# Performance work log

Measured on AMD Instinct MI355X. Metric: run time of the kernel, lower is better.

Reference implementation:

```python
import jax, jax.numpy as jnp
import numpy as np

HIDDEN = 2048
HEADS = 16
HEAD_DIM = HIDDEN // HEADS
BATCH = 2
SEQ = 2048
ROPE_BASE = 10000.0


def _rope_cos_sin(seq_len, head_dim, dtype):
    inv_freq = 1.0 / (ROPE_BASE ** (jnp.arange(0, head_dim, 2, dtype=jnp.float32) / head_dim))
    t = jnp.arange(seq_len, dtype=jnp.float32)
    freqs = jnp.outer(t, inv_freq)                 # [S, D/2]
    emb = jnp.concatenate([freqs, freqs], axis=-1)  # [S, D]
    return jnp.cos(emb).astype(dtype), jnp.sin(emb).astype(dtype)


def _rotate_half(x):
    x1, x2 = jnp.split(x, 2, axis=-1)
    return jnp.concatenate([-x2, x1], axis=-1)


def setup_inputs() -> dict:
    key = jax.random.key(0)
    ks = jax.random.split(key, 5)
    scale = 1.0 / np.sqrt(HIDDEN)
    return {
        "x": jax.random.normal(ks[0], (BATCH, SEQ, HIDDEN), dtype=jnp.float32),
        "Wq": jax.random.normal(ks[1], (HIDDEN, HIDDEN), dtype=jnp.float32) * scale,
        "Wk": jax.random.normal(ks[2], (HIDDEN, HIDDEN), dtype=jnp.float32) * scale,
        "Wv": jax.random.normal(ks[3], (HIDDEN, HIDDEN), dtype=jnp.float32) * scale,
        "Wo": jax.random.normal(ks[4], (HIDDEN, HIDDEN), dtype=jnp.float32) * scale,
    }


def reference(x, Wq, Wk, Wv, Wo):
    B, S, H = x.shape
    # projections (torch Linear: y = x @ W.T)
    q = jnp.einsum('bsh,oh->bso', x, Wq).reshape(B, S, HEADS, HEAD_DIM).transpose(0, 2, 1, 3)
    k = jnp.einsum('bsh,oh->bso', x, Wk).reshape(B, S, HEADS, HEAD_DIM).transpose(0, 2, 1, 3)
    v = jnp.einsum('bsh,oh->bso', x, Wv).reshape(B, S, HEADS, HEAD_DIM).transpose(0, 2, 1, 3)
    # RoPE
    cos, sin = _rope_cos_sin(S, HEAD_DIM, x.dtype)  # [S, D]
    cos = cos[None, None]  # [1,1,S,D]
    sin = sin[None, None]
    q = q * cos + _rotate_half(q) * sin
    k = k * cos + _rotate_half(k) * sin
    # attention scores [B, H, S, S]
    scale = HEAD_DIM ** -0.5
    scores = jnp.einsum('bhqd,bhkd->bhqk', q, k) * scale
    causal = jnp.triu(jnp.ones((S, S), dtype=bool), k=1)  # kv_len==seq -> diagonal=1
    scores = jnp.where(causal[None, None], -jnp.inf, scores)
    attn = jax.nn.softmax(scores.astype(jnp.float32), axis=-1).astype(q.dtype)
    # dropout is identity in eval mode
    out = jnp.einsum('bhqk,bhkd->bhqd', attn, v)  # [B,H,S,D]
    out = out.transpose(0, 2, 1, 3).reshape(B, S, H)
    return jnp.einsum('bsh,oh->bso', out, Wo)
```

## Files before the change

kernel.cpp:

```cpp
#include <hip/hip_runtime.h>
#include <hip/hip_bf16.h>
#include <cstdint>
#include <cstddef>

constexpr int HIDDEN = 2048;
constexpr int HEADS  = 16;
constexpr int HD     = 128;
constexpr int BATCH  = 2;
constexpr int SEQ    = 2048;
constexpr int MROWS  = BATCH * SEQ;

typedef __attribute__((ext_vector_type(8))) short bf16x8;
typedef __attribute__((ext_vector_type(4))) float f32x4;
typedef __attribute__((ext_vector_type(4))) unsigned u32x4;

constexpr float QSCALE = 0.08838834764831845f * 1.4426950408889634f;

__device__ __forceinline__ unsigned short f2bf(float f) {
  union { float f; unsigned int u; } c; c.f = f;
  unsigned int r = c.u + 0x7FFFu + ((c.u >> 16) & 1u);
  return (unsigned short)(r >> 16);
}
__device__ __forceinline__ float bf2f(unsigned short u) {
  union { unsigned int u; float f; } c; c.u = ((unsigned int)u) << 16;
  return c.f;
}

__device__ __forceinline__ void gload_lds16(const void* g, void* l) {
  __builtin_amdgcn_global_load_lds(
      (const __attribute__((address_space(1))) void*)g,
      (__attribute__((address_space(3))) void*)l, 16, 0, 0);
}

__global__ void k_cvt_all(const float* __restrict__ x,
                          const float* __restrict__ w0, const float* __restrict__ w1,
                          const float* __restrict__ w2, const float* __restrict__ w3,
                          unsigned short* __restrict__ out) {
  constexpr int N4X = MROWS * HIDDEN / 4;
  constexpr int N4W = HIDDEN * HIDDEN / 4;
  int idx = blockIdx.x * 256 + threadIdx.x;
  const float* src;
  int off;
  if (idx < N4X) { src = x; off = idx; }
  else {
    int j = idx - N4X;
    int seg = j >> 20;
    off = j & (N4W - 1);
    src = (seg == 0) ? w0 : (seg == 1) ? w1 : (seg == 2) ? w2 : w3;
  }
  float4 v = reinterpret_cast<const float4*>(src)[off];
  ushort4 o;
  o.x = f2bf(v.x); o.y = f2bf(v.y); o.z = f2bf(v.z); o.w = f2bf(v.w);
  reinterpret_cast<ushort4*>(out)[idx] = o;
}

constexpr int GK  = 2048;
constexpr int GNT = GK / 64;

template<int MODE, int BM, int BN>
__global__ __launch_bounds__(512)
__attribute__((amdgpu_waves_per_eu(2)))
void k_gemm256(const unsigned short* __restrict__ A,
               const unsigned short* __restrict__ Bm,
               void* __restrict__ Cout) {
  constexpr int ABYTES = BM * 64 * 2;
  constexpr int BBYTES = BN * 64 * 2;
  constexpr int AG = BM / 64;
  constexpr int BG = BN / 64;
  constexpr int G  = AG + BG;
  constexpr int MI = BM / 32;
  constexpr int NI = BN / 64;

  __shared__ char lds[2 * (ABYTES + BBYTES)];
  char* ldsA = lds;
  char* ldsB = lds + 2 * ABYTES;

  const int t    = threadIdx.x;
  const int lane = t & 63;
  const int w    = t >> 6;
  const int wr   = w >> 2;
  const int wc   = w & 3;
  const int l15  = lane & 15, lg = lane >> 4;

  const int orig = blockIdx.x;
  const int wg   = (orig & 7) * 32 + (orig >> 3);
  const int m0   = (wg >> 4) * BM;
  const int n0   = (wg & 15) * BN;

  const int rowA = t >> 3;
  const int xsel = ((t & 7) ^ (rowA & 7)) * 8;
  const unsigned short* aS = A  + (size_t)(m0 + rowA) * GK + xsel;
  const unsigned short* bS = Bm + (size_t)(n0 + rowA) * GK + xsel;
  char* aD = ldsA + t * 16;
  char* bD = ldsB + t * 16;

#define STAGEG(buf, kt) do {                                       \
    const unsigned short* ap = aS + (kt) * 64;                     \
    const unsigned short* bp = bS + (kt) * 64;                     \
    char* ad = aD + (buf) * ABYTES;                                \
    char* bd = bD + (buf) * BBYTES;                                \
    _Pragma("unroll")                                              \
    for (int g = 0; g < AG; ++g)                                   \
      gload_lds16(ap + (size_t)g * 64 * GK, ad + g * 8192);        \
    _Pragma("unroll")                                              \
    for (int g = 0; g < BG; ++g)                                   \
      gload_lds16(bp + (size_t)g * 64 * GK, bd + g * 8192);        \
  } while (0)

  const int xr  = (l15 & 7) << 4;
  const int vo0 = (lg * 16) ^ xr;
  const int vo1 = (64 + lg * 16) ^ xr;
  const char* aR = ldsA + wr * (BM / 2) * 128 + l15 * 128;
  const char* bR = ldsB + wc * (BN / 4) * 128 + l15 * 128;

  f32x4 acc[MI][NI];
#pragma unroll
  for (int mi = 0; mi < MI; ++mi)
#pragma unroll
    for (int ni = 0; ni < NI; ++ni)
#pragma unroll
      for (int r = 0; r < 4; ++r) acc[mi][ni][r] = 0.f;

  STAGEG(0, 0);
  STAGEG(1, 1);
  asm volatile("s_waitcnt vmcnt(%0)" :: "i"(G) : "memory");
  __builtin_amdgcn_s_barrier();
  asm volatile("" ::: "memory");

#pragma unroll 1
  for (int kt = 0; kt < GNT; ++kt) {
    const int buf = kt & 1;
    const char* a = aR + buf * ABYTES;
    const char* b = bR + buf * BBYTES;

    bf16x8 af0[MI], bf0[NI];
#pragma unroll
    for (int mi = 0; mi < MI; ++mi)
      af0[mi] = *reinterpret_cast<const bf16x8*>(a + mi * 2048 + vo0);
#pragma unroll
    for (int ni = 0; ni < NI; ++ni)
      bf0[ni] = *reinterpret_cast<const bf16x8*>(b + ni * 2048 + vo0);
    __builtin_amdgcn_s_setprio(1);
#pragma unroll
    for (int mi = 0; mi < MI; ++mi)
#pragma unroll
      for (int ni = 0; ni < NI; ++ni)
        acc[mi][ni] = __builtin_amdgcn_mfma_f32_16x16x32_bf16(af0[mi], bf0[ni], acc[mi][ni], 0, 0, 0);
    __builtin_amdgcn_s_setprio(0);

    bf16x8 af1[MI], bf1[NI];
#pragma unroll
    for (int mi = 0; mi < MI; ++mi)
      af1[mi] = *reinterpret_cast<const bf16x8*>(a + mi * 2048 + vo1);
#pragma unroll
    for (int ni = 0; ni < NI; ++ni)
      bf1[ni] = *reinterpret_cast<const bf16x8*>(b + ni * 2048 + vo1);

    asm volatile("s_waitcnt lgkmcnt(0)" ::: "memory");
    __builtin_amdgcn_s_barrier();
    asm volatile("" ::: "memory");

    if (kt < GNT - 2) STAGEG(buf, kt + 2);

    __builtin_amdgcn_s_setprio(1);
#pragma unroll
    for (int mi = 0; mi < MI; ++mi)
#pragma unroll
      for (int ni = 0; ni < NI; ++ni)
        acc[mi][ni] = __builtin_amdgcn_mfma_f32_16x16x32_bf16(af1[mi], bf1[ni], acc[mi][ni], 0, 0, 0);
    __builtin_amdgcn_s_setprio(0);

    if (kt < GNT - 2) asm volatile("s_waitcnt vmcnt(%0)" :: "i"(G) : "memory");
    else              asm volatile("s_waitcnt vmcnt(0)" ::: "memory");
    __builtin_amdgcn_s_barrier();
    asm volatile("" ::: "memory");
  }
#undef STAGEG

  if (MODE == 0) {
    float* xch = reinterpret_cast<float*>(lds);
    const int lid = w * 64 + lane;
    const int pid = (w ^ 1) * 64 + lane;
#pragma unroll
    for (int half = 0; half < 2; ++half) {
      __syncthreads();
#pragma unroll
      for (int mi4 = 0; mi4 < 4; ++mi4)
#pragma unroll
        for (int ni = 0; ni < NI; ++ni)
#pragma unroll
          for (int r = 0; r < 4; ++r)
            xch[(mi4 * 16 + ni * 4 + r) * 512 + lid] = acc[half * 4 + mi4][ni][r];
      __syncthreads();
#pragma unroll
      for (int mi4 = 0; mi4 < 4; ++mi4) {
#pragma unroll
        for (int ni = 0; ni < NI; ++ni) {
          const int col  = n0 + wc * 64 + ni * 16 + l15;
          const float invf = exp2f((float)(col & 63) * -0.20762050593046868f);
#pragma unroll
          for (int r = 0; r < 4; ++r) {
            int row = m0 + wr * 128 + (half * 4 + mi4) * 16 + lg * 4 + r;
            int s = row & (SEQ - 1);
            float own = acc[half * 4 + mi4][ni][r];
            float oth = xch[(mi4 * 16 + ni * 4 + r) * 512 + pid];
            float sn, cs;
            __sincosf((float)s * invf, &sn, &cs);
            float outv = (wc & 1) ? (own * cs + oth * sn) : (own * cs - oth * sn);
            int bb = row >> 11;
            int which = col >> 11;
            int hc = col & 2047;
            int h = hc >> 7, d = hc & (HD - 1);
            if (which == 0) outv *= QSCALE;
            size_t addr = (size_t)which * ((size_t)MROWS * HIDDEN)
                        + ((size_t)(bb * HEADS + h) * SEQ + s) * HD + d;
            reinterpret_cast<unsigned short*>(Cout)[addr] = f2bf(outv);
          }
        }
      }
    }
  } else {
#pragma unroll
    for (int mi = 0; mi < MI; ++mi) {
#pragma unroll
      for (int ni = 0; ni < NI; ++ni) {
#pragma unroll
        for (int r = 0; r < 4; ++r) {
          int row = m0 + wr * (BM / 2) + mi * 16 + lg * 4 + r;
          int col = n0 + wc * (BN / 4) + ni * 16 + l15;
          float v = acc[mi][ni][r];
          if (MODE == 2) {
            reinterpret_cast<float*>(Cout)[(size_t)row * 2048 + col] = v;
          } else {
            int h = row >> 7, d = row & (HD - 1);
            int bb = col >> 11, s = col & (SEQ - 1);
            size_t addr = ((size_t)(bb * HEADS + h) * HD + d) * SEQ + s;
            reinterpret_cast<unsigned short*>(Cout)[addr] = f2bf(v);
          }
        }
      }
    }
  }
}

constexpr int QB  = 128;
constexpr int KVB = 64;
constexpr int NQT = SEQ / QB;

__global__ __launch_bounds__(512)
__attribute__((amdgpu_waves_per_eu(4, 4)))
void k_attn(const unsigned short* __restrict__ Q,
            const unsigned short* __restrict__ Kk,
            const unsigned short* __restrict__ Vt,
            unsigned short* __restrict__ O) {
  __shared__ char lds[2 * 16384 + 2 * 16384];
  char* Ks = lds;
  char* Vs = lds + 2 * 16384;

  const int t    = threadIdx.x;
  const int lane = t & 63;
  const int w    = t >> 6;
  const int l15  = lane & 15, lg = lane >> 4;

  const int lin     = blockIdx.x + 16 * blockIdx.y;
  const int pos     = lin >> 3;
  const int logical = (lin & 7) * 64 + pos;
  const int bh      = logical >> 4;
  const int qt0     = logical & 15;
  const int qt      = (pos < 32) ? qt0 : (15 - qt0);
  const int b  = bh >> 4, h = bh & 15;
  const int q0b  = qt * QB;
  const int q0w  = q0b + w * 16;
  const int qw_hi = q0w + 15;

  const unsigned short* Qb = Q  + (size_t)bh * SEQ * HD;
  const unsigned short* Kb = Kk + (size_t)bh * SEQ * HD;
  const unsigned short* Vb = Vt + (size_t)bh * HD * SEQ;

  bf16x8 qf[4];
#pragma unroll
  for (int c = 0; c < 4; ++c)
    qf[c] = *reinterpret_cast<const bf16x8*>(Qb + (size_t)(q0w + l15) * HD + c * 32 + lg * 8);

  float m = -1e30f, lpart = 0.f;
  f32x4 oacc[8];
#pragma unroll
  for (int dt = 0; dt < 8; ++dt)
#pragma unroll
    for (int r = 0; r < 4; ++r) oacc[dt][r] = 0.f;

  const int sp     = t * 16;
  const int srow   = sp >> 8;
  const int scolb  = (sp & 255) ^ ((srow & 7) << 4);
  const unsigned short* ksrc2 = Kb + (size_t)srow * HD + (scolb >> 1);
  char* kdst2 = Ks + sp;

  const int vrow  = t >> 3;
  const int vcolb = ((t & 7) << 4) ^ ((vrow & 7) << 4);
  const unsigned short* vsrc = Vb + (size_t)vrow * SEQ + (vcolb >> 1);
  char* vdst = Vs + t * 16;

  const int nb = q0b / KVB + 2;

  gload_lds16(ksrc2, kdst2);
  gload_lds16(ksrc2 + (size_t)32 * HD, kdst2 + 8192);
  gload_lds16(vsrc, vdst);
  gload_lds16(vsrc + (size_t)64 * SEQ, vdst + 8192);

  int cur = 0;
  for (int kb = 0; kb < nb; ++kb) {
    const int kv0 = kb * KVB;
    if (kb + 1 < nb) {
      const int nxt = kv0 + KVB;
      char* nk = kdst2 + (cur ^ 1) * 16384;
      char* nv = vdst  + (cur ^ 1) * 16384;
      gload_lds16(ksrc2 + (size_t)nxt * HD, nk);
      gload_lds16(ksrc2 + (size_t)(nxt + 32) * HD, nk + 8192);
      gload_lds16(vsrc + nxt, nv);
      gload_lds16(vsrc + (size_t)64 * SEQ + nxt, nv + 8192);
      asm volatile("s_waitcnt vmcnt(4)" ::: "memory");
    } else {
      asm volatile("s_waitcnt vmcnt(0)" ::: "memory");
    }
    __builtin_amdgcn_s_barrier();
    asm volatile("" ::: "memory");

    if (kv0 <= qw_hi) {
      const char* Kc = Ks + cur * 16384;
      const char* Vc = Vs + cur * 16384;
      f32x4 sc[4];
#pragma unroll
      for (int tt = 0; tt < 4; ++tt)
#pragma unroll
        for (int r = 0; r < 4; ++r) sc[tt][r] = 0.f;
      __builtin_amdgcn_s_setprio(1);
#pragma unroll
      for (int tt = 0; tt < 4; ++tt) {
        const int kr = tt * 16 + l15;
        const int xr = (kr & 7) << 4;
#pragma unroll
        for (int c = 0; c < 4; ++c) {
          bf16x8 kf = *reinterpret_cast<const bf16x8*>(
              Kc + kr * 256 + ((c * 64 + lg * 16) ^ xr));
          sc[tt] = __builtin_amdgcn_mfma_f32_16x16x32_bf16(kf, qf[c], sc[tt], 0, 0, 0);
        }
      }
      __builtin_amdgcn_s_setprio(0);

      const bool full = (kv0 + KVB - 1 <= q0w);
      const int qg = q0w + l15;
      if (!full) {
        const int kvb = kv0 + lg * 4;
#pragma unroll
        for (int tt = 0; tt < 4; ++tt)
#pragma unroll
          for (int r = 0; r < 4; ++r)
            if (kvb + tt * 16 + r > qg) sc[tt][r] = -1e30f;
      }
      float pm01 = fmaxf(fmaxf(sc[0][0], sc[0][1]), fmaxf(sc[0][2], sc[0][3]));
      float pm11 = fmaxf(fmaxf(sc[1][0], sc[1][1]), fmaxf(sc[1][2], sc[1][3]));
      float pm21 = fmaxf(fmaxf(sc[2][0], sc[2][1]), fmaxf(sc[2][2], sc[2][3]));
      float pm31 = fmaxf(fmaxf(sc[3][0], sc[3][1]), fmaxf(sc[3][2], sc[3][3]));
      float pm = fmaxf(fmaxf(pm01, pm11), fmaxf(pm21, pm31));
      if (__any(pm > m + 11.5f)) {
        float pmr = pm;
        pmr = fmaxf(pmr, __shfl_xor(pmr, 16));
        pmr = fmaxf(pmr, __shfl_xor(pmr, 32));
        float mn = fmaxf(m, pmr);
        float al = exp2f(m - mn);
        lpart *= al;
#pragma unroll
        for (int r = 0; r < 4; ++r) {
          float alr = __shfl(al, lg * 4 + r, 16);
#pragma unroll
          for (int dt = 0; dt < 8; ++dt) oacc[dt][r] *= alr;
        }
        m = mn;
      }
      float p[4][4];
      float ps = 0.f;
#pragma unroll
      for (int tt = 0; tt < 4; ++tt)
#pragma unroll
        for (int r = 0; r < 4; ++r) {
          p[tt][r] = exp2f(sc[tt][r] - m);
          ps += p[tt][r];
        }
      lpart += ps;

      unsigned cc[4][2];
#pragma unroll
      for (int tt = 0; tt < 4; ++tt) {
        asm("v_cvt_pk_bf16_f32 %0, %1, %2" : "=v"(cc[tt][0]) : "v"(p[tt][0]), "v"(p[tt][1]));
        asm("v_cvt_pk_bf16_f32 %0, %1, %2" : "=v"(cc[tt][1]) : "v"(p[tt][2]), "v"(p[tt][3]));
      }
      u32x4 u0, u1;
      {
        unsigned a0 = cc[0][0], b0 = cc[1][0];
        asm("v_permlane32_swap_b32 %0, %1" : "+v"(a0), "+v"(b0));
        asm("v_permlane16_swap_b32 %0, %1" : "+v"(a0), "+v"(b0));
        unsigned a1 = cc[0][1], b1 = cc[1][1];
        asm("v_permlane32_swap_b32 %0, %1" : "+v"(a1), "+v"(b1));
        asm("v_permlane16_swap_b32 %0, %1" : "+v"(a1), "+v"(b1));
        u0[0] = a0; u0[1] = a1; u0[2] = b0; u0[3] = b1;
        unsigned a2 = cc[2][0], b2 = cc[3][0];
        asm("v_permlane32_swap_b32 %0, %1" : "+v"(a2), "+v"(b2));
        asm("v_permlane16_swap_b32 %0, %1" : "+v"(a2), "+v"(b2));
        unsigned a3 = cc[2][1], b3 = cc[3][1];
        asm("v_permlane32_swap_b32 %0, %1" : "+v"(a3), "+v"(b3));
        asm("v_permlane16_swap_b32 %0, %1" : "+v"(a3), "+v"(b3));
        u1[0] = a2; u1[1] = a3; u1[2] = b2; u1[3] = b3;
      }
      bf16x8 pa0 = __builtin_bit_cast(bf16x8, u0);
      bf16x8 pa1 = __builtin_bit_cast(bf16x8, u1);

      const int xv = (l15 & 7) << 4;
      __builtin_amdgcn_s_setprio(1);
#pragma unroll
      for (int dt = 0; dt < 8; ++dt) {
        const char* vrl = Vc + (dt * 16 + l15) * 128;
        bf16x8 vf0 = *reinterpret_cast<const bf16x8*>(vrl + ((lg * 16) ^ xv));
        bf16x8 vf1 = *reinterpret_cast<const bf16x8*>(vrl + ((64 + lg * 16) ^ xv));
        oacc[dt] = __builtin_amdgcn_mfma_f32_16x16x32_bf16(pa0, vf0, oacc[dt], 0, 0, 0);
        oacc[dt] = __builtin_amdgcn_mfma_f32_16x16x32_bf16(pa1, vf1, oacc[dt], 0, 0, 0);
      }
      __builtin_amdgcn_s_setprio(0);
    }
    __builtin_amdgcn_s_barrier();
    asm volatile("" ::: "memory");
    cur ^= 1;
  }

  float ls = lpart;
  ls += __shfl_xor(ls, 16);
  ls += __shfl_xor(ls, 32);
  float inv = 1.0f / ls;
  float invr[4];
#pragma unroll
  for (int r = 0; r < 4; ++r) invr[r] = __shfl(inv, lg * 4 + r, 16);
#pragma unroll
  for (int dt = 0; dt < 8; ++dt) {
#pragma unroll
    for (int r = 0; r < 4; ++r) {
      int qg = q0w + lg * 4 + r;
      int dv = dt * 16 + l15;
      O[((size_t)(b * SEQ + qg) * HEADS + h) * HD + dv] = f2bf(oacc[dt][r] * invr[r]);
    }
  }
}

extern "C" void kernel_launch(void* const* d_in, const int* in_sizes, int n_in,
                              void* d_out, int out_size, void* d_ws, size_t ws_size,
                              hipStream_t stream) {
  (void)in_sizes; (void)n_in; (void)out_size; (void)ws_size;
  const float* x  = (const float*)d_in[0];
  const float* Wq = (const float*)d_in[1];
  const float* Wk = (const float*)d_in[2];
  const float* Wv = (const float*)d_in[3];
  const float* Wo = (const float*)d_in[4];
  float* out = (float*)d_out;

  unsigned short* xb  = (unsigned short*)d_ws;
  unsigned short* wqb = xb  + (size_t)MROWS * HIDDEN;
  unsigned short* wkb = wqb + (size_t)HIDDEN * HIDDEN;
  unsigned short* wvb = wkb + (size_t)HIDDEN * HIDDEN;
  unsigned short* wob = wvb + (size_t)HIDDEN * HIDDEN;
  unsigned short* Qb  = wob + (size_t)HIDDEN * HIDDEN;
  unsigned short* Kb  = Qb  + (size_t)MROWS * HIDDEN;
  unsigned short* Vtb = Kb  + (size_t)MROWS * HIDDEN;
  unsigned short* Ob  = Vtb + (size_t)MROWS * HIDDEN;
  (void)wkb;

  constexpr int CVT_THREADS = (MROWS * HIDDEN + 4 * HIDDEN * HIDDEN) / 4;
  k_cvt_all<<<CVT_THREADS / 256, 256, 0, stream>>>(x, Wq, Wk, Wv, Wo, xb);

  k_gemm256<0, 256, 256><<<256, 512, 0, stream>>>(xb, wqb, Qb);
  k_gemm256<3, 128, 256><<<256, 512, 0, stream>>>(wvb, xb, Vtb);

  k_attn<<<dim3(SEQ / QB, BATCH * HEADS), 512, 0, stream>>>(Qb, Kb, Vtb, Ob);

  k_gemm256<2, 256, 128><<<256, 512, 0, stream>>>(Ob, wob, out);
}
```

Measured before the change: 228.4 us.

## Remap QKV GEMM B-fragment columns so each wave holds both RoPE halves

In the QKV projection GEMM (MODE 0), the B-operand LDS read offsets change so each wave's NI column fragments pair dimension d with d+64 of the same head. The RoPE rotation can then be done entirely in registers, which removes the LDS exchange of accumulators between partner waves and its two barriers per half. Sin/cos is also computed once per row and reused for both halves. The correctness of this remapping depends on the tile geometry (BN, wave layout) matching the assumed offsets.

```diff
diff --git a/kernel.cpp b/kernel.cpp
--- a/kernel.cpp
+++ b/kernel.cpp
@@ -111,7 +111,9 @@
   const int vo0 = (lg * 16) ^ xr;
   const int vo1 = (64 + lg * 16) ^ xr;
   const char* aR = ldsA + wr * (BM / 2) * 128 + l15 * 128;
-  const char* bR = ldsB + wc * (BN / 4) * 128 + l15 * 128;
+  const char* bR = (MODE == 0) ? (ldsB + wc * 2048 + l15 * 128)
+                               : (ldsB + wc * (BN / 4) * 128 + l15 * 128);
+#define BOFF(ni) ((MODE == 0) ? (((ni) & 1) * 8192 + ((ni) >> 1) * 16384) : ((ni) * 2048))
 
   f32x4 acc[MI][NI];
 #pragma unroll
@@ -139,7 +141,7 @@
       af0[mi] = *reinterpret_cast<const bf16x8*>(a + mi * 2048 + vo0);
 #pragma unroll
     for (int ni = 0; ni < NI; ++ni)
-      bf0[ni] = *reinterpret_cast<const bf16x8*>(b + ni * 2048 + vo0);
+      bf0[ni] = *reinterpret_cast<const bf16x8*>(b + BOFF(ni) + vo0);
     __builtin_amdgcn_s_setprio(1);
 #pragma unroll
     for (int mi = 0; mi < MI; ++mi)
@@ -154,7 +156,7 @@
       af1[mi] = *reinterpret_cast<const bf16x8*>(a + mi * 2048 + vo1);
 #pragma unroll
     for (int ni = 0; ni < NI; ++ni)
-      bf1[ni] = *reinterpret_cast<const bf16x8*>(b + ni * 2048 + vo1);
+      bf1[ni] = *reinterpret_cast<const bf16x8*>(b + BOFF(ni) + vo1);
 
     asm volatile("s_waitcnt lgkmcnt(0)" ::: "memory");
     __builtin_amdgcn_s_barrier();
@@ -176,46 +178,34 @@
     asm volatile("" ::: "memory");
   }
 #undef STAGEG
+#undef BOFF
 
   if (MODE == 0) {
-    float* xch = reinterpret_cast<float*>(lds);
-    const int lid = w * 64 + lane;
-    const int pid = (w ^ 1) * 64 + lane;
-#pragma unroll
-    for (int half = 0; half < 2; ++half) {
-      __syncthreads();
-#pragma unroll
-      for (int mi4 = 0; mi4 < 4; ++mi4)
-#pragma unroll
-        for (int ni = 0; ni < NI; ++ni)
-#pragma unroll
-          for (int r = 0; r < 4; ++r)
-            xch[(mi4 * 16 + ni * 4 + r) * 512 + lid] = acc[half * 4 + mi4][ni][r];
-      __syncthreads();
-#pragma unroll
-      for (int mi4 = 0; mi4 < 4; ++mi4) {
-#pragma unroll
-        for (int ni = 0; ni < NI; ++ni) {
-          const int col  = n0 + wc * 64 + ni * 16 + l15;
-          const float invf = exp2f((float)(col & 63) * -0.20762050593046868f);
-#pragma unroll
-          for (int r = 0; r < 4; ++r) {
-            int row = m0 + wr * 128 + (half * 4 + mi4) * 16 + lg * 4 + r;
-            int s = row & (SEQ - 1);
-            float own = acc[half * 4 + mi4][ni][r];
-            float oth = xch[(mi4 * 16 + ni * 4 + r) * 512 + pid];
-            float sn, cs;
-            __sincosf((float)s * invf, &sn, &cs);
-            float outv = (wc & 1) ? (own * cs + oth * sn) : (own * cs - oth * sn);
-            int bb = row >> 11;
-            int which = col >> 11;
-            int hc = col & 2047;
-            int h = hc >> 7, d = hc & (HD - 1);
-            if (which == 0) outv *= QSCALE;
-            size_t addr = (size_t)which * ((size_t)MROWS * HIDDEN)
-                        + ((size_t)(bb * HEADS + h) * SEQ + s) * HD + d;
-            reinterpret_cast<unsigned short*>(Cout)[addr] = f2bf(outv);
-          }
+    const int dp = wc * 16 + l15;
+    const float invf = exp2f((float)dp * -0.20762050593046868f);
+    const int colbase = n0 + wc * 16 + l15;
+#pragma unroll
+    for (int mi = 0; mi < MI; ++mi) {
+#pragma unroll
+      for (int r = 0; r < 4; ++r) {
+        int row = m0 + wr * 128 + mi * 16 + lg * 4 + r;
+        int s  = row & (SEQ - 1);
+        int bb = row >> 11;
+        float sn, cs;
+        __sincosf((float)s * invf, &sn, &cs);
+#pragma unroll
+        for (int p = 0; p < 2; ++p) {
+          float lo = acc[mi][p * 2][r], hi = acc[mi][p * 2 + 1][r];
+          float olo = lo * cs - hi * sn;
+          float ohi = hi * cs + lo * sn;
+          int col   = colbase + p * 128;
+          int which = col >> 11;
+          int h     = (col & 2047) >> 7;
+          if (which == 0) { olo *= QSCALE; ohi *= QSCALE; }
+          size_t base = (size_t)which * ((size_t)MROWS * HIDDEN)
+                      + ((size_t)(bb * HEADS + h) * SEQ + s) * HD + dp;
+          reinterpret_cast<unsigned short*>(Cout)[base]      = f2bf(olo);
+          reinterpret_cast<unsigned short*>(Cout)[base + 64] = f2bf(ohi);
         }
       }
     }
```

Result: no change. 225.8 us (median of 3 runs) (-1.1%).
